# Kernel optimization log

Hardware: AMD Instinct MI355X
Metric: run time of the kernel (lower is better)

The kernel has to match this reference:

```python
import jax, jax.numpy as jnp
import numpy as np
from jax import lax

C = 128
N_HEADS = 4
HEAD_D = C // N_HEADS
EXP = 2  # FFN expansion


def _ln_c(x, g, b, eps):
    # LayerNorm over channel dim of NCHW (equivalent to to_3d -> LN(c) -> to_4d)
    m = jnp.mean(x, axis=1, keepdims=True)
    v = jnp.mean((x - m) ** 2, axis=1, keepdims=True)
    return (x - m) / jnp.sqrt(v + eps) * g[None, :, None, None] + b[None, :, None, None]


def _conv1x1(x, w, b):
    # w: (out, in)
    return jnp.einsum('bchw,oc->bohw', x, w) + b[None, :, None, None]


def _dwconv(x, w, b):
    # depthwise conv, w: (Cg, 1, k, k), stride 1, SAME padding
    y = lax.conv_general_dilated(
        x, w, window_strides=(1, 1), padding='SAME',
        dimension_numbers=('NCHW', 'OIHW', 'NCHW'),
        feature_group_count=x.shape[1])
    return y + b[None, :, None, None]


def setup_inputs() -> dict:
    key = jax.random.key(0)
    ks = jax.random.split(key, 24)
    s = 0.05
    hid = C
    e = EXP * C
    inp = {
        'feats1': jax.random.normal(ks[0], (2, C, 64, 256), jnp.float32),
        'feats2': jax.random.normal(ks[1], (2, C, 64, 256), jnp.float32),
        # attention norms
        'an_g': jnp.ones((C,), jnp.float32), 'an_b': jnp.zeros((C,), jnp.float32),
        'anc_g': jnp.ones((C,), jnp.float32), 'anc_b': jnp.zeros((C,), jnp.float32),
        # qkv / out 1x1 convs
        'wq': jax.random.normal(ks[2], (hid, C), jnp.float32) * s,
        'bq': jnp.zeros((hid,), jnp.float32),
        'wkv': jax.random.normal(ks[3], (2 * hid, C), jnp.float32) * s,
        'bkv': jnp.zeros((2 * hid,), jnp.float32),
        'wo': jax.random.normal(ks[4], (C, hid), jnp.float32) * s,
        'bo': jnp.zeros((C,), jnp.float32),
        # FFN
        'fn_g': jnp.ones((C,), jnp.float32), 'fn_b': jnp.zeros((C,), jnp.float32),
        'w_in': jax.random.normal(ks[5], (e, C), jnp.float32) * s,
        'b_in': jnp.zeros((e,), jnp.float32),
        'w_dw3': jax.random.normal(ks[6], (e, 1, 3, 3), jnp.float32) * s,
        'b_dw3': jnp.zeros((e,), jnp.float32),
        'w_dw5': jax.random.normal(ks[7], (e, 1, 5, 5), jnp.float32) * s,
        'b_dw5': jnp.zeros((e,), jnp.float32),
        'w_dw7': jax.random.normal(ks[8], (e, 1, 7, 7), jnp.float32) * s,
        'b_dw7': jnp.zeros((e,), jnp.float32),
        'w_pw': jax.random.normal(ks[9], (e, 3 * e), jnp.float32) * s,
        'b_pw': jnp.zeros((e,), jnp.float32),
        'w_out': jax.random.normal(ks[10], (C, e), jnp.float32) * s,
        'b_out': jnp.zeros((C,), jnp.float32),
    }
    return inp


def reference(feats1, feats2, an_g, an_b, anc_g, anc_b, wq, bq, wkv, bkv, wo, bo,
              fn_g, fn_b, w_in, b_in, w_dw3, b_dw3, w_dw5, b_dw5, w_dw7, b_dw7,
              w_pw, b_pw, w_out, b_out):
    eps = 1e-6
    hid = C
    n, d = N_HEADS, HEAD_D
    scale = d ** (-0.5)

    # bi-directional cross attention: doubled batch
    cat1 = jnp.concatenate([feats1, feats2], axis=0)  # (B, C, H, W)
    cat2 = jnp.concatenate([feats2, feats1], axis=0)
    B, _, H, W = cat1.shape

    # pre-norm (separate norms for query and context streams)
    x1 = _ln_c(cat1, an_g, an_b, eps)
    x2 = _ln_c(cat2, anc_g, anc_b, eps)

    q = _conv1x1(x1, wq, bq)                     # (B, hid, H, W)
    kv = _conv1x1(x2, wkv, bkv)
    k, v = kv[:, :hid], kv[:, hid:]

    qh = q.reshape(B, n, d, H, W)
    kh = k.reshape(B, n, d, H, W)
    vh = v.reshape(B, n, d, H, W)

    # per-row (epipolar) attention over width
    sim = jnp.einsum('bndhi,bndhj->bnhij', qh, kh) * scale  # (B, n, H, W, W)
    # sink competition renorm
    attn = jax.nn.softmax(sim, axis=-1) + eps
    attn = attn / jnp.sum(attn, axis=-1, keepdims=True)

    o = jnp.einsum('bnhij,bndhj->bndhi', attn, vh).reshape(B, hid, H, W)
    o = _conv1x1(o, wo, bo)
    cat1 = cat1 + o

    # multiscale depthwise-conv FFN (receptive_aug='conv')
    y = _ln_c(cat1, fn_g, fn_b, 1e-5)
    y = jax.nn.silu(_conv1x1(y, w_in, b_in))     # (B, 2C, H, W)
    f3 = _dwconv(y, w_dw3, b_dw3)
    f5 = _dwconv(y, w_dw5, b_dw5)
    f7 = _dwconv(y, w_dw7, b_dw7)
    y = y + jax.nn.silu(_conv1x1(jnp.concatenate([f3, f5, f7], axis=1), w_pw, b_pw))
    y = _conv1x1(y, w_out, b_out)
    cat1 = cat1 + y

    half = B // 2
    return cat1[:half], cat1[half:]
```

## Files before the change

### kernel.cpp

```cpp
#include <hip/hip_runtime.h>

typedef unsigned short u16;
typedef unsigned int u32;

constexpr int H_ = 64;
constexpr int W_ = 256;
constexpr int HW_ = H_ * W_;

typedef __bf16 bf16x8 __attribute__((ext_vector_type(8)));
typedef float f32x4 __attribute__((ext_vector_type(4)));

__device__ __forceinline__ float bf2f(u16 v) { return __uint_as_float(((u32)v) << 16); }
__device__ __forceinline__ u16 f2bf(float f) {
  u32 x = __float_as_uint(f);
  u32 r = (x + 0x7fffu + ((x >> 16) & 1u)) >> 16;
  return (u16)r;
}
__device__ __forceinline__ float lo2f(u32 p) { return __uint_as_float(p << 16); }
__device__ __forceinline__ float hi2f(u32 p) { return __uint_as_float(p & 0xffff0000u); }
__device__ __forceinline__ void unpack8(uint4 v, float* f) {
  f[0] = lo2f(v.x); f[1] = hi2f(v.x);
  f[2] = lo2f(v.y); f[3] = hi2f(v.y);
  f[4] = lo2f(v.z); f[5] = hi2f(v.z);
  f[6] = lo2f(v.w); f[7] = hi2f(v.w);
}
__device__ __forceinline__ bf16x8 as_bf16x8(uint4 v) {
  union { uint4 u; bf16x8 b; } x; x.u = v; return x.b;
}
__device__ __forceinline__ int swz(int p, int c) { return c ^ (((p >> 3) & 3) << 3); }

constexpr int NT = 26;
constexpr int ELEMS_PER_BLK = 4096;
struct CvtArgs {
  const void* src[NT];
  u32 dst_off[NT];
  u32 n[NT];
  u32 blk_start[NT];
};

__global__ void convert_all(CvtArgs a, u16* __restrict__ dst) {
  const u32 bid = blockIdx.x;
  int ti = 0;
#pragma unroll
  for (int k = 1; k < NT; ++k) if (a.blk_start[k] <= bid) ti = k;
  const u32 e0 = (bid - a.blk_start[ti]) * ELEMS_PER_BLK;
  const u32 n = a.n[ti];
  u32 hi = e0 + ELEMS_PER_BLK; if (hi > n) hi = n;
  const float* sp = (const float*)a.src[ti];
  u16* d = dst + a.dst_off[ti];
  for (u32 i = e0 + threadIdx.x; i < hi; i += 256) d[i] = f2bf(sp[i]);
}

template <int CIN, int COUT>
__launch_bounds__(256)
__global__ void gemm1x1_ln(const u16* __restrict__ xA, const u16* __restrict__ xB,
                           const u16* __restrict__ w, const u16* __restrict__ bias,
                           const u16* __restrict__ lng, const u16* __restrict__ lnb,
                           float lneps, u16* __restrict__ out) {
  constexpr int POS = 64;
  constexpr int PITCH = CIN + 8;
  constexpr int MT = COUT / 64;
  __shared__ __align__(16) u16 xs[POS * PITCH];
  __shared__ float red1[256], red2[256], stm[64], str[64];
  const int t = threadIdx.x;
  const int b = blockIdx.y;
  const int pos0 = blockIdx.x * POS;

  const u16* basep = (b >= 2) ? xB : xA;
  const int bb = (b < 2) ? b : b - 2;
  const u16* xb16 = basep + (size_t)bb * CIN * HW_;

  constexpr int NLOAD = CIN * POS / 8;
  for (int idx = t; idx < NLOAD; idx += 256) {
    const int c = idx / (POS / 8);
    const int p8 = (idx % (POS / 8)) * 8;
    uint4 v = *(const uint4*)(xb16 + (size_t)c * HW_ + pos0 + p8);
    const int csw = swz(p8, c);
    u16* row = xs + p8 * PITCH + csw;
    row[0]         = (u16)v.x; row[PITCH]     = (u16)(v.x >> 16);
    row[2 * PITCH] = (u16)v.y; row[3 * PITCH] = (u16)(v.y >> 16);
    row[4 * PITCH] = (u16)v.z; row[5 * PITCH] = (u16)(v.z >> 16);
    row[6 * PITCH] = (u16)v.w; row[7 * PITCH] = (u16)(v.w >> 16);
  }
  __syncthreads();

  {
    const int p = t & 63, part = t >> 6;
    const int xorp = ((p >> 3) & 3) << 3;
    float s = 0.f, sq = 0.f;
#pragma unroll
    for (int k = 0; k < 32; k += 8) {
      uint4 v = *(const uint4*)(xs + p * PITCH + ((part * 32 + k) ^ xorp));
      float f[8]; unpack8(v, f);
#pragma unroll
      for (int j = 0; j < 8; ++j) { s += f[j]; sq += f[j] * f[j]; }
    }
    red1[part * 64 + p] = s; red2[part * 64 + p] = sq;
    __syncthreads();
    if (t < 64) {
      float ss = red1[t] + red1[64 + t] + red1[128 + t] + red1[192 + t];
      float qq = red2[t] + red2[64 + t] + red2[128 + t] + red2[192 + t];
      float m = ss * (1.0f / CIN);
      float var = qq * (1.0f / CIN) - m * m;
      var = var < 0.f ? 0.f : var;
      stm[t] = m; str[t] = rsqrtf(var + lneps);
    }
    __syncthreads();
    const float m = stm[p], r = str[p];
#pragma unroll
    for (int k = 0; k < 32; k += 8) {
      const int c = part * 32 + k;
      uint4 v = *(const uint4*)(xs + p * PITCH + (c ^ xorp));
      float f[8]; unpack8(v, f);
      u32 pk[4];
#pragma unroll
      for (int j = 0; j < 8; j += 2) {
        float g0 = bf2f(lng[c + j]), be0 = bf2f(lnb[c + j]);
        float g1 = bf2f(lng[c + j + 1]), be1 = bf2f(lnb[c + j + 1]);
        u16 lo = f2bf((f[j] - m) * r * g0 + be0);
        u16 hi = f2bf((f[j + 1] - m) * r * g1 + be1);
        pk[j >> 1] = (u32)lo | ((u32)hi << 16);
      }
      uint4 ov; ov.x = pk[0]; ov.y = pk[1]; ov.z = pk[2]; ov.w = pk[3];
      *(uint4*)(xs + p * PITCH + (c ^ xorp)) = ov;
    }
    __syncthreads();
  }

  const int lane = t & 63, wv = t >> 6;
  const int lo16 = lane & 15, quad = lane >> 4;
  const int orow0 = wv * MT * 16;
  const int qrow = quad * 4;

  f32x4 acc[MT][4];
#pragma unroll
  for (int mt = 0; mt < MT; ++mt) {
#pragma unroll
    for (int r = 0; r < 4; ++r) {
      const float bv = bf2f(bias[orow0 + mt * 16 + qrow + r]);
#pragma unroll
      for (int nt = 0; nt < 4; ++nt) acc[mt][nt][r] = bv;
    }
  }

  const u16* xb[4];
#pragma unroll
  for (int nt = 0; nt < 4; ++nt) {
    const int row = nt * 16 + lo16;
    xb[nt] = xs + row * PITCH + (quad * 8 ^ ((((row >> 3) & 3)) << 3));
  }
  const u16* wl = w + (size_t)(orow0 + lo16) * CIN + quad * 8;

#pragma unroll 2
  for (int kc = 0; kc < CIN / 32; ++kc) {
    const int c0 = kc * 32;
    bf16x8 bfr[4];
#pragma unroll
    for (int nt = 0; nt < 4; ++nt)
      bfr[nt] = as_bf16x8(*(const uint4*)(xb[nt] + c0));
#pragma unroll
    for (int mt = 0; mt < MT; ++mt) {
      bf16x8 afr = as_bf16x8(*(const uint4*)(wl + (size_t)mt * 16 * CIN + c0));
#pragma unroll
      for (int nt = 0; nt < 4; ++nt)
        acc[mt][nt] = __builtin_amdgcn_mfma_f32_16x16x32_bf16(afr, bfr[nt], acc[mt][nt], 0, 0, 0);
    }
  }

#pragma unroll
  for (int mt = 0; mt < MT; ++mt) {
#pragma unroll
    for (int nt = 0; nt < 4; ++nt) {
#pragma unroll
      for (int r = 0; r < 4; ++r) {
        const int o = orow0 + mt * 16 + qrow + r;
        const int p = pos0 + nt * 16 + lo16;
        out[((size_t)b * COUT + o) * HW_ + p] = f2bf(acc[mt][nt][r]);
      }
    }
  }
}

__launch_bounds__(256)
__global__ void attn_mfma(const u16* __restrict__ qb, const u16* __restrict__ kvb,
                          u16* __restrict__ ob) {
  constexpr int PA = 40;
  constexpr int PJ = 264;
  __shared__ __align__(16) u16 kT[256 * PA];
  __shared__ __align__(16) u16 vT[32 * PJ];
  __shared__ __align__(16) u16 PlO[4 * 16 * PJ];
  const int t = threadIdx.x;
  const int h = blockIdx.x, n = blockIdx.y, b = blockIdx.z;
  const size_t qbase = ((size_t)(b * 128 + n * 32)) * HW_ + (size_t)h * W_;
  const size_t kbase = ((size_t)(b * 256 + n * 32)) * HW_ + (size_t)h * W_;
  const size_t vbase = ((size_t)(b * 256 + 128 + n * 32)) * HW_ + (size_t)h * W_;

#pragma unroll
  for (int d8 = 0; d8 < 4; ++d8) {
    u32 pk[4];
#pragma unroll
    for (int j = 0; j < 4; ++j) {
      u32 lo = kvb[kbase + (size_t)(d8 * 8 + 2 * j) * HW_ + t];
      u32 hi = kvb[kbase + (size_t)(d8 * 8 + 2 * j + 1) * HW_ + t];
      pk[j] = lo | (hi << 16);
    }
    *(uint4*)(kT + t * PA + d8 * 8) = make_uint4(pk[0], pk[1], pk[2], pk[3]);
  }
#pragma unroll
  for (int k = 0; k < 16; ++k) {
    const int idx = k * 256 + t;
    const int d = idx >> 7, p2 = (idx & 127) * 2;
    u32 v = *(const u32*)(kvb + vbase + (size_t)d * HW_ + p2);
    *(u32*)(vT + d * PJ + p2) = v;
  }
  __syncthreads();

  const int lane = t & 63, wv = t >> 6;
  const int lo16 = lane & 15, quad = lane >> 4;
  const float scale = 0.17677669529663687f;
  const float renorm = 1.0f / (1.0f + 256.0f * 1e-6f);
  const float addc = 1e-6f * renorm;
  u16* Pw = PlO + wv * 16 * PJ;

  f32x4 oacc[4][2];
  for (int ii = 0; ii < 4; ++ii) {
    const int i0 = ii * 64 + wv * 16;
    u16 qr[8];
#pragma unroll
    for (int j = 0; j < 8; ++j)
      qr[j] = qb[qbase + (size_t)(quad * 8 + j) * HW_ + i0 + lo16];
    bf16x8 qa;
#pragma unroll
    for (int j = 0; j < 8; ++j) qa[j] = *(__bf16*)&qr[j];
    f32x4 s[16];
#pragma unroll
    for (int jt = 0; jt < 16; ++jt) {
      bf16x8 kb = as_bf16x8(*(const uint4*)(kT + (jt * 16 + lo16) * PA + quad * 8));
      f32x4 z = {0.f, 0.f, 0.f, 0.f};
      s[jt] = __builtin_amdgcn_mfma_f32_16x16x32_bf16(qa, kb, z, 0, 0, 0);
    }
#pragma unroll
    for (int r = 0; r < 4; ++r) {
      float sum = 0.f;
#pragma unroll
      for (int jt = 0; jt < 16; ++jt) {
        float e = __expf(s[jt][r] * scale);
        s[jt][r] = e; sum += e;
      }
#pragma unroll
      for (int off = 1; off <= 8; off <<= 1) sum += __shfl_xor(sum, off, 64);
      const float inv2 = renorm / sum;
#pragma unroll
      for (int jt = 0; jt < 16; ++jt)
        Pw[(quad * 4 + r) * PJ + jt * 16 + lo16] = f2bf(fmaf(s[jt][r], inv2, addc));
    }
    f32x4 o0 = {0.f, 0.f, 0.f, 0.f}, o1 = {0.f, 0.f, 0.f, 0.f};
#pragma unroll
    for (int kt = 0; kt < 8; ++kt) {
      bf16x8 pa = as_bf16x8(*(const uint4*)(Pw + lo16 * PJ + kt * 32 + quad * 8));
      bf16x8 v0 = as_bf16x8(*(const uint4*)(vT + lo16 * PJ + kt * 32 + quad * 8));
      bf16x8 v1 = as_bf16x8(*(const uint4*)(vT + (16 + lo16) * PJ + kt * 32 + quad * 8));
      o0 = __builtin_amdgcn_mfma_f32_16x16x32_bf16(pa, v0, o0, 0, 0, 0);
      o1 = __builtin_amdgcn_mfma_f32_16x16x32_bf16(pa, v1, o1, 0, 0, 0);
    }
    oacc[ii][0] = o0; oacc[ii][1] = o1;
  }
  __syncthreads();
  u16* Ob = PlO;
#pragma unroll
  for (int ii = 0; ii < 4; ++ii) {
    const int i0 = ii * 64 + wv * 16;
#pragma unroll
    for (int r = 0; r < 4; ++r) {
      Ob[(i0 + quad * 4 + r) * PA + lo16] = f2bf(oacc[ii][0][r]);
      Ob[(i0 + quad * 4 + r) * PA + 16 + lo16] = f2bf(oacc[ii][1][r]);
    }
  }
  __syncthreads();
  for (int d = 0; d < 32; ++d) ob[qbase + (size_t)d * HW_ + t] = Ob[t * PA + d];
}

__launch_bounds__(256)
__global__ void fused_proj_ffn(const u16* __restrict__ obf,
                               const u16* __restrict__ wo, const u16* __restrict__ bo_,
                               const float* __restrict__ f1, const float* __restrict__ f2,
                               const u16* __restrict__ fng, const u16* __restrict__ fnb,
                               const u16* __restrict__ w_in, const u16* __restrict__ b_in,
                               u16* __restrict__ cat1b, u16* __restrict__ yb) {
  constexpr int PITCH = 136;
  __shared__ __align__(16) u16 xs[64 * PITCH];
  __shared__ float red1[256], red2[256], stm[64], str[64];
  const int t = threadIdx.x;
  const int b = blockIdx.y;
  const int pos0 = blockIdx.x * 64;
  const u16* xb16 = obf + (size_t)b * 128 * HW_;

  for (int idx = t; idx < 1024; idx += 256) {
    const int c = idx >> 3, p8 = (idx & 7) * 8;
    uint4 v = *(const uint4*)(xb16 + (size_t)c * HW_ + pos0 + p8);
    const int csw = swz(p8, c);
    u16* row = xs + p8 * PITCH + csw;
    row[0]         = (u16)v.x; row[PITCH]     = (u16)(v.x >> 16);
    row[2 * PITCH] = (u16)v.y; row[3 * PITCH] = (u16)(v.y >> 16);
    row[4 * PITCH] = (u16)v.z; row[5 * PITCH] = (u16)(v.z >> 16);
    row[6 * PITCH] = (u16)v.w; row[7 * PITCH] = (u16)(v.w >> 16);
  }
  __syncthreads();

  const int lane = t & 63, wv = t >> 6;
  const int lo16 = lane & 15, quad = lane >> 4, qrow = quad * 4;
  const u16* xb[4];
#pragma unroll
  for (int nt = 0; nt < 4; ++nt) {
    const int row = nt * 16 + lo16;
    xb[nt] = xs + row * PITCH + (quad * 8 ^ ((((row >> 3) & 3)) << 3));
  }

  const int orow0 = wv * 32;
  f32x4 acc1[2][4];
#pragma unroll
  for (int mt = 0; mt < 2; ++mt)
#pragma unroll
    for (int r = 0; r < 4; ++r) {
      const float bv = bf2f(bo_[orow0 + mt * 16 + qrow + r]);
#pragma unroll
      for (int nt = 0; nt < 4; ++nt) acc1[mt][nt][r] = bv;
    }
  const u16* wl1 = wo + (size_t)(orow0 + lo16) * 128 + quad * 8;
#pragma unroll
  for (int kc = 0; kc < 4; ++kc) {
    const int c0 = kc * 32;
    bf16x8 bfr[4];
#pragma unroll
    for (int nt = 0; nt < 4; ++nt) bfr[nt] = as_bf16x8(*(const uint4*)(xb[nt] + c0));
#pragma unroll
    for (int mt = 0; mt < 2; ++mt) {
      bf16x8 afr = as_bf16x8(*(const uint4*)(wl1 + (size_t)mt * 16 * 128 + c0));
#pragma unroll
      for (int nt = 0; nt < 4; ++nt)
        acc1[mt][nt] = __builtin_amdgcn_mfma_f32_16x16x32_bf16(afr, bfr[nt], acc1[mt][nt], 0, 0, 0);
    }
  }
  __syncthreads();

  {
    const int bl = (b < 2) ? b : b - 2;
    const float* rb = (b < 2) ? f1 : f2;
#pragma unroll
    for (int mt = 0; mt < 2; ++mt)
#pragma unroll
      for (int nt = 0; nt < 4; ++nt)
#pragma unroll
        for (int r = 0; r < 4; ++r) {
          const int o = orow0 + mt * 16 + qrow + r;
          const int p = nt * 16 + lo16;
          float v = acc1[mt][nt][r] + rb[((size_t)bl * 128 + o) * HW_ + pos0 + p];
          const u16 bv = f2bf(v);
          cat1b[((size_t)b * 128 + o) * HW_ + pos0 + p] = bv;
          xs[p * PITCH + swz(p, o)] = bv;
        }
  }
  __syncthreads();

  {
    const int p = t & 63, part = t >> 6;
    const int xorp = ((p >> 3) & 3) << 3;
    float s = 0.f, sq = 0.f;
#pragma unroll
    for (int k = 0; k < 32; k += 8) {
      uint4 v = *(const uint4*)(xs + p * PITCH + ((part * 32 + k) ^ xorp));
      float f[8]; unpack8(v, f);
#pragma unroll
      for (int j = 0; j < 8; ++j) { s += f[j]; sq += f[j] * f[j]; }
    }
    red1[part * 64 + p] = s; red2[part * 64 + p] = sq;
    __syncthreads();
    if (t < 64) {
      float ss = red1[t] + red1[64 + t] + red1[128 + t] + red1[192 + t];
      float qq = red2[t] + red2[64 + t] + red2[128 + t] + red2[192 + t];
      float m = ss * (1.0f / 128.0f);
      float var = qq * (1.0f / 128.0f) - m * m;
      var = var < 0.f ? 0.f : var;
      stm[t] = m; str[t] = rsqrtf(var + 1e-5f);
    }
    __syncthreads();
    const float m = stm[p], r = str[p];
#pragma unroll
    for (int k = 0; k < 32; k += 8) {
      const int c = part * 32 + k;
      uint4 v = *(const uint4*)(xs + p * PITCH + (c ^ xorp));
      float f[8]; unpack8(v, f);
      u32 pk[4];
#pragma unroll
      for (int j = 0; j < 8; j += 2) {
        float g0 = bf2f(fng[c + j]), be0 = bf2f(fnb[c + j]);
        float g1 = bf2f(fng[c + j + 1]), be1 = bf2f(fnb[c + j + 1]);
        u16 lo = f2bf((f[j] - m) * r * g0 + be0);
        u16 hi = f2bf((f[j + 1] - m) * r * g1 + be1);
        pk[j >> 1] = (u32)lo | ((u32)hi << 16);
      }
      uint4 ov; ov.x = pk[0]; ov.y = pk[1]; ov.z = pk[2]; ov.w = pk[3];
      *(uint4*)(xs + p * PITCH + (c ^ xorp)) = ov;
    }
    __syncthreads();
  }

  const int orow2 = wv * 64;
  f32x4 acc2[4][4];
#pragma unroll
  for (int mt = 0; mt < 4; ++mt)
#pragma unroll
    for (int r = 0; r < 4; ++r) {
      const float bv = bf2f(b_in[orow2 + mt * 16 + qrow + r]);
#pragma unroll
      for (int nt = 0; nt < 4; ++nt) acc2[mt][nt][r] = bv;
    }
  const u16* wl2 = w_in + (size_t)(orow2 + lo16) * 128 + quad * 8;
#pragma unroll
  for (int kc = 0; kc < 4; ++kc) {
    const int c0 = kc * 32;
    bf16x8 bfr[4];
#pragma unroll
    for (int nt = 0; nt < 4; ++nt) bfr[nt] = as_bf16x8(*(const uint4*)(xb[nt] + c0));
#pragma unroll
    for (int mt = 0; mt < 4; ++mt) {
      bf16x8 afr = as_bf16x8(*(const uint4*)(wl2 + (size_t)mt * 16 * 128 + c0));
#pragma unroll
      for (int nt = 0; nt < 4; ++nt)
        acc2[mt][nt] = __builtin_amdgcn_mfma_f32_16x16x32_bf16(afr, bfr[nt], acc2[mt][nt], 0, 0, 0);
    }
  }
#pragma unroll
  for (int mt = 0; mt < 4; ++mt)
#pragma unroll
    for (int nt = 0; nt < 4; ++nt)
#pragma unroll
      for (int r = 0; r < 4; ++r) {
        const int o = orow2 + mt * 16 + qrow + r;
        const int p = nt * 16 + lo16;
        float v = acc2[mt][nt][r];
        v = v / (1.0f + __expf(-v));
        yb[((size_t)b * 256 + o) * HW_ + pos0 + p] = f2bf(v);
      }
}

__launch_bounds__(512, 4)
__global__ void fused_pw_out(const u16* __restrict__ fbase, size_t f_stride,
                             const u16* __restrict__ w_pw, const u16* __restrict__ b_pw,
                             const u16* __restrict__ yb,
                             const u16* __restrict__ w_out, const u16* __restrict__ b_out,
                             const u16* __restrict__ cat1b, float* __restrict__ outp,
                             int b_off) {
  constexpr int SP = 136;
  constexpr int P2 = 264;
  constexpr int NCHK = 6;
  __shared__ __align__(16) u16 sbuf[2][64 * SP];
  u16* y2 = &sbuf[0][0];

  const int t = threadIdx.x;
  const int bo2 = (int)blockIdx.y + b_off;
  const int pos0 = blockIdx.x * 64;
  const u16* xf = fbase + (size_t)blockIdx.y * f_stride;

  const int lane = t & 63, wv = t >> 6;
  const int lo16 = lane & 15, quad = lane >> 4, qrow = quad * 4;

  const int c_s0 = t >> 3;
  const int c_s1 = c_s0 + 64;
  const int p8_s = (t & 7) * 8;
  const size_t g_off = pos0 + p8_s;

  uint4 pf0, pf1;
  pf0 = *(const uint4*)(xf + (size_t)c_s0 * HW_ + g_off);
  pf1 = *(const uint4*)(xf + (size_t)c_s1 * HW_ + g_off);
  {
    u16* r0 = sbuf[0] + p8_s * SP + swz(p8_s, c_s0);
    r0[0]      = (u16)pf0.x; r0[SP]     = (u16)(pf0.x >> 16);
    r0[2 * SP] = (u16)pf0.y; r0[3 * SP] = (u16)(pf0.y >> 16);
    r0[4 * SP] = (u16)pf0.z; r0[5 * SP] = (u16)(pf0.z >> 16);
    r0[6 * SP] = (u16)pf0.w; r0[7 * SP] = (u16)(pf0.w >> 16);
    u16* r1 = sbuf[0] + p8_s * SP + swz(p8_s, c_s1);
    r1[0]      = (u16)pf1.x; r1[SP]     = (u16)(pf1.x >> 16);
    r1[2 * SP] = (u16)pf1.y; r1[3 * SP] = (u16)(pf1.y >> 16);
    r1[4 * SP] = (u16)pf1.z; r1[5 * SP] = (u16)(pf1.z >> 16);
    r1[6 * SP] = (u16)pf1.w; r1[7 * SP] = (u16)(pf1.w >> 16);
  }
  pf0 = *(const uint4*)(xf + (size_t)(128 + c_s0) * HW_ + g_off);
  pf1 = *(const uint4*)(xf + (size_t)(128 + c_s1) * HW_ + g_off);

  const int orow1 = wv * 32;
  f32x4 acc[2][4];
#pragma unroll
  for (int mt = 0; mt < 2; ++mt)
#pragma unroll
    for (int r = 0; r < 4; ++r) {
      const float bv = bf2f(b_pw[orow1 + mt * 16 + qrow + r]);
#pragma unroll
      for (int nt = 0; nt < 4; ++nt) acc[mt][nt][r] = bv;
    }
  int xoff[4];
#pragma unroll
  for (int nt = 0; nt < 4; ++nt) {
    const int row = nt * 16 + lo16;
    xoff[nt] = row * SP + (quad * 8 ^ ((((row >> 3) & 3)) << 3));
  }
  const u16* wl1 = w_pw + (size_t)(orow1 + lo16) * 768 + quad * 8;

  __syncthreads();

  for (int ch = 0; ch < NCHK; ++ch) {
    if (ch + 1 < NCHK) {
      u16* dst = sbuf[(ch + 1) & 1];
      u16* r0 = dst + p8_s * SP + swz(p8_s, c_s0);
      r0[0]      = (u16)pf0.x; r0[SP]     = (u16)(pf0.x >> 16);
      r0[2 * SP] = (u16)pf0.y; r0[3 * SP] = (u16)(pf0.y >> 16);
      r0[4 * SP] = (u16)pf0.z; r0[5 * SP] = (u16)(pf0.z >> 16);
      r0[6 * SP] = (u16)pf0.w; r0[7 * SP] = (u16)(pf0.w >> 16);
      u16* r1 = dst + p8_s * SP + swz(p8_s, c_s1);
      r1[0]      = (u16)pf1.x; r1[SP]     = (u16)(pf1.x >> 16);
      r1[2 * SP] = (u16)pf1.y; r1[3 * SP] = (u16)(pf1.y >> 16);
      r1[4 * SP] = (u16)pf1.z; r1[5 * SP] = (u16)(pf1.z >> 16);
      r1[6 * SP] = (u16)pf1.w; r1[7 * SP] = (u16)(pf1.w >> 16);
    }
    if (ch + 2 < NCHK) {
      pf0 = *(const uint4*)(xf + (size_t)((ch + 2) * 128 + c_s0) * HW_ + g_off);
      pf1 = *(const uint4*)(xf + (size_t)((ch + 2) * 128 + c_s1) * HW_ + g_off);
    }
    const u16* xs = sbuf[ch & 1];
    const u16* wch = wl1 + ch * 128;
#pragma unroll
    for (int kc = 0; kc < 4; ++kc) {
      const int c0 = kc * 32;
      bf16x8 bfr[4];
#pragma unroll
      for (int nt = 0; nt < 4; ++nt)
        bfr[nt] = as_bf16x8(*(const uint4*)(xs + xoff[nt] + c0));
#pragma unroll
      for (int mt = 0; mt < 2; ++mt) {
        bf16x8 afr = as_bf16x8(*(const uint4*)(wch + (size_t)mt * 16 * 768 + c0));
#pragma unroll
        for (int nt = 0; nt < 4; ++nt)
          acc[mt][nt] = __builtin_amdgcn_mfma_f32_16x16x32_bf16(afr, bfr[nt], acc[mt][nt], 0, 0, 0);
      }
    }
    __syncthreads();
  }

#pragma unroll
  for (int mt = 0; mt < 2; ++mt)
#pragma unroll
    for (int nt = 0; nt < 4; ++nt)
#pragma unroll
      for (int r = 0; r < 4; ++r) {
        const int o = orow1 + mt * 16 + qrow + r;
        const int p = nt * 16 + lo16;
        float v = acc[mt][nt][r];
        v = v / (1.0f + __expf(-v));
        v += bf2f(yb[((size_t)bo2 * 256 + o) * HW_ + pos0 + p]);
        y2[p * P2 + swz(p, o)] = f2bf(v);
      }
  __syncthreads();

  int x2off[4];
#pragma unroll
  for (int nt = 0; nt < 4; ++nt) {
    const int row = nt * 16 + lo16;
    x2off[nt] = row * P2 + (quad * 8 ^ ((((row >> 3) & 3)) << 3));
  }
  const int orow2 = wv * 16;
  f32x4 acc2[4];
#pragma unroll
  for (int r = 0; r < 4; ++r) {
    const float bv = bf2f(b_out[orow2 + qrow + r]);
#pragma unroll
    for (int nt = 0; nt < 4; ++nt) acc2[nt][r] = bv;
  }
  const u16* wl2 = w_out + (size_t)(orow2 + lo16) * 256 + quad * 8;
#pragma unroll
  for (int kc = 0; kc < 8; ++kc) {
    const int c0 = kc * 32;
    bf16x8 bfr[4];
#pragma unroll
    for (int nt = 0; nt < 4; ++nt) bfr[nt] = as_bf16x8(*(const uint4*)(y2 + x2off[nt] + c0));
    bf16x8 afr = as_bf16x8(*(const uint4*)(wl2 + c0));
#pragma unroll
    for (int nt = 0; nt < 4; ++nt)
      acc2[nt] = __builtin_amdgcn_mfma_f32_16x16x32_bf16(afr, bfr[nt], acc2[nt], 0, 0, 0);
  }
#pragma unroll
  for (int nt = 0; nt < 4; ++nt)
#pragma unroll
    for (int r = 0; r < 4; ++r) {
      const int o = orow2 + qrow + r;
      const int p = nt * 16 + lo16;
      const size_t gidx = ((size_t)bo2 * 128 + o) * HW_ + pos0 + p;
      outp[gidx] = acc2[nt][r] + bf2f(cat1b[gidx]);
    }
}

__launch_bounds__(256)
__global__ void dwconv_kernel(const u16* __restrict__ yB,
                              const u16* __restrict__ w3, const u16* __restrict__ b3,
                              const u16* __restrict__ w5, const u16* __restrict__ b5,
                              const u16* __restrict__ w7, const u16* __restrict__ b7,
                              u16* __restrict__ fB) {
  constexpr int LW = 70, LH = 14, LP = 72;
  __shared__ u16 tile[LH * LP];
  __shared__ float wf7[49], wf5[25], wf3[9];
  const int t = threadIdx.x;
  const int c = blockIdx.y;
  const int bz = blockIdx.z;
  const int tw = blockIdx.x & 3, th = blockIdx.x >> 2;
  const int w0 = tw * 64, h0 = th * 8;
  const u16* src = yB + ((size_t)bz * 256 + c) * HW_;

  if (t < 49) wf7[t] = bf2f(w7[c * 49 + t]);
  if (t >= 64 && t < 89) wf5[t - 64] = bf2f(w5[c * 25 + (t - 64)]);
  if (t >= 96 && t < 105) wf3[t - 96] = bf2f(w3[c * 9 + (t - 96)]);

  for (int idx = t; idx < LH * LW; idx += 256) {
    const int r = idx / LW, cc = idx - r * LW;
    const int gh = h0 + r - 3, gw = w0 + cc - 3;
    u16 v = 0;
    if (gh >= 0 && gh < H_ && gw >= 0 && gw < W_) v = src[gh * W_ + gw];
    tile[r * LP + cc] = v;
  }
  __syncthreads();

  const int x0 = (t & 31) * 2;
  const int hh = t >> 5;
  float a3x = 0.f, a3y = 0.f, a5x = 0.f, a5y = 0.f, a7x = 0.f, a7y = 0.f;
#pragma unroll
  for (int rr = 0; rr < 7; ++rr) {
    const u16* trow = tile + (hh + rr) * LP + x0;
    float f[10];
#pragma unroll
    for (int k = 0; k < 5; ++k) {
      u32 v = *(const u32*)(trow + 2 * k);
      f[2 * k] = lo2f(v); f[2 * k + 1] = hi2f(v);
    }
#pragma unroll
    for (int dx = 0; dx < 7; ++dx) {
      const float wv = wf7[rr * 7 + dx];
      a7x += wv * f[dx]; a7y += wv * f[dx + 1];
    }
    if (rr >= 1 && rr <= 5) {
#pragma unroll
      for (int dx = 0; dx < 5; ++dx) {
        const float wv = wf5[(rr - 1) * 5 + dx];
        a5x += wv * f[dx + 1]; a5y += wv * f[dx + 2];
      }
    }
    if (rr >= 2 && rr <= 4) {
#pragma unroll
      for (int dx = 0; dx < 3; ++dx) {
        const float wv = wf3[(rr - 2) * 3 + dx];
        a3x += wv * f[dx + 2]; a3y += wv * f[dx + 3];
      }
    }
  }
  const float B3v = bf2f(b3[c]), B5v = bf2f(b5[c]), B7v = bf2f(b7[c]);
  const size_t o0 = (size_t)bz * 768 * HW_ + (size_t)c * HW_ + (size_t)(h0 + hh) * W_ + (w0 + x0);
  *(u32*)(fB + o0) = (u32)f2bf(a3x + B3v) | ((u32)f2bf(a3y + B3v) << 16);
  *(u32*)(fB + o0 + (size_t)256 * HW_) = (u32)f2bf(a5x + B5v) | ((u32)f2bf(a5y + B5v) << 16);
  *(u32*)(fB + o0 + (size_t)512 * HW_) = (u32)f2bf(a7x + B7v) | ((u32)f2bf(a7y + B7v) << 16);
}

extern "C" void kernel_launch(void* const* d_in, const int* in_sizes, int n_in,
                              void* d_out, int out_size, void* d_ws, size_t ws_size,
                              hipStream_t stream) {
  (void)out_size; (void)n_in;
  char* ws = (char*)d_ws;
  const size_t MB = 1ull << 20;

  u16* arena = (u16*)ws;
  CvtArgs ca;
  u32 off = 0, blk = 0;
  u32 aoff[NT];
  for (int i = 0; i < NT; ++i) {
    ca.src[i] = d_in[i];
    ca.n[i] = (u32)in_sizes[i];
    ca.dst_off[i] = off;
    aoff[i] = off;
    ca.blk_start[i] = blk;
    off += (ca.n[i] + 15u) & ~15u;
    blk += (ca.n[i] + ELEMS_PER_BLK - 1) / ELEMS_PER_BLK;
  }
  const u32 total_blocks = blk;

  const u16* f1c   = arena + aoff[0];
  const u16* f2c   = arena + aoff[1];
  const u16* an_g  = arena + aoff[2];
  const u16* an_b  = arena + aoff[3];
  const u16* anc_g = arena + aoff[4];
  const u16* anc_b = arena + aoff[5];
  const u16* wq    = arena + aoff[6];
  const u16* bq    = arena + aoff[7];
  const u16* wkv   = arena + aoff[8];
  const u16* bkv   = arena + aoff[9];
  const u16* wo    = arena + aoff[10];
  const u16* bo_   = arena + aoff[11];
  const u16* fn_g  = arena + aoff[12];
  const u16* fn_b  = arena + aoff[13];
  const u16* w_in  = arena + aoff[14];
  const u16* b_in  = arena + aoff[15];
  const u16* w3    = arena + aoff[16];
  const u16* b3    = arena + aoff[17];
  const u16* w5    = arena + aoff[18];
  const u16* b5    = arena + aoff[19];
  const u16* w7    = arena + aoff[20];
  const u16* b7    = arena + aoff[21];
  const u16* w_pw  = arena + aoff[22];
  const u16* b_pw  = arena + aoff[23];
  const u16* w_out = arena + aoff[24];
  const u16* b_out = arena + aoff[25];

  u16* cat1b  = (u16*)(ws + 18 * MB);
  u16* qb     = (u16*)(ws + 34 * MB);
  u16* kvb    = (u16*)(ws + 50 * MB);
  u16* obf    = (u16*)(ws + 82 * MB);
  u16* yb     = (u16*)(ws + 34 * MB);
  u16* fbuf   = (u16*)(ws + 66 * MB);
  float* outp = (float*)d_out;
  const bool big = ws_size >= 168 * MB;

  dim3 blk256(256);
  dim3 blk512(512);
  convert_all<<<total_blocks, 256, 0, stream>>>(ca, arena);

  gemm1x1_ln<128, 128><<<dim3(HW_ / 64, 4), blk256, 0, stream>>>(
      f1c, f2c, wq, bq, an_g, an_b, 1e-6f, qb);
  gemm1x1_ln<128, 256><<<dim3(HW_ / 64, 4), blk256, 0, stream>>>(
      f2c, f1c, wkv, bkv, anc_g, anc_b, 1e-6f, kvb);
  attn_mfma<<<dim3(64, 4, 4), blk256, 0, stream>>>(qb, kvb, obf);
  fused_proj_ffn<<<dim3(HW_ / 64, 4), blk256, 0, stream>>>(
      obf, wo, bo_, (const float*)d_in[0], (const float*)d_in[1],
      fn_g, fn_b, w_in, b_in, cat1b, yb);
  if (big) {
    dwconv_kernel<<<dim3(32, 256, 4), blk256, 0, stream>>>(yb, w3, b3, w5, b5, w7, b7, fbuf);
    fused_pw_out<<<dim3(HW_ / 64, 4), blk512, 0, stream>>>(
        fbuf, (size_t)768 * HW_, w_pw, b_pw, yb, w_out, b_out, cat1b, outp, 0);
  } else {
    for (int b = 0; b < 4; ++b) {
      dwconv_kernel<<<dim3(32, 256, 1), blk256, 0, stream>>>(
          yb + (size_t)b * 256 * HW_, w3, b3, w5, b5, w7, b7, fbuf);
      fused_pw_out<<<dim3(HW_ / 64, 1), blk512, 0, stream>>>(
          fbuf, 0, w_pw, b_pw, yb, w_out, b_out, cat1b, outp, b);
    }
  }
}
```

Baseline: 376.9 us.

## Widen depthwise conv tiles to full rows with 8 outputs per thread

The depthwise 3/5/7 conv kernel now tiles full 256-wide rows (8 rows per block) and stores the halo tile in shared memory as fp32 instead of bf16. Each thread computes 8 adjacent outputs per scale instead of 2, using vectorized float4 LDS reads of input and padded weights, and writes 16-byte stores. This cuts halo overhead, per-element bf16 unpacking and LDS traffic per output, and improves store width. In exchange the grid shrinks fourfold, register pressure rises with 24 accumulators, and the fp32 tile uses more LDS, which may lower occupancy.

After: 438.9 us. +16.4%, slower.

```diff
diff --git a/kernel.cpp b/kernel.cpp
--- a/kernel.cpp
+++ b/kernel.cpp
@@ -604,66 +604,99 @@
                               const u16* __restrict__ w5, const u16* __restrict__ b5,
                               const u16* __restrict__ w7, const u16* __restrict__ b7,
                               u16* __restrict__ fB) {
-  constexpr int LW = 70, LH = 14, LP = 72;
-  __shared__ u16 tile[LH * LP];
-  __shared__ float wf7[49], wf5[25], wf3[9];
+  constexpr int TP = 264;
+  __shared__ __align__(16) float tile[14 * TP];
+  __shared__ __align__(16) float wf7p[56];
+  __shared__ __align__(16) float wf5p[40];
+  __shared__ __align__(16) float wf3p[12];
   const int t = threadIdx.x;
   const int c = blockIdx.y;
   const int bz = blockIdx.z;
-  const int tw = blockIdx.x & 3, th = blockIdx.x >> 2;
-  const int w0 = tw * 64, h0 = th * 8;
+  const int h0 = blockIdx.x * 8;
   const u16* src = yB + ((size_t)bz * 256 + c) * HW_;
 
-  if (t < 49) wf7[t] = bf2f(w7[c * 49 + t]);
-  if (t >= 64 && t < 89) wf5[t - 64] = bf2f(w5[c * 25 + (t - 64)]);
-  if (t >= 96 && t < 105) wf3[t - 96] = bf2f(w3[c * 9 + (t - 96)]);
-
-  for (int idx = t; idx < LH * LW; idx += 256) {
-    const int r = idx / LW, cc = idx - r * LW;
-    const int gh = h0 + r - 3, gw = w0 + cc - 3;
-    u16 v = 0;
-    if (gh >= 0 && gh < H_ && gw >= 0 && gw < W_) v = src[gh * W_ + gw];
-    tile[r * LP + cc] = v;
-  }
-  __syncthreads();
-
-  const int x0 = (t & 31) * 2;
+  if (t < 56) {
+    const int rr = t >> 3, dx = t & 7;
+    wf7p[t] = (dx < 7) ? bf2f(w7[c * 49 + rr * 7 + dx]) : 0.f;
+  } else if (t >= 64 && t < 104) {
+    const int i = t - 64, rr = i >> 3, dx = i & 7;
+    wf5p[i] = (dx < 5) ? bf2f(w5[c * 25 + rr * 5 + dx]) : 0.f;
+  } else if (t >= 112 && t < 124) {
+    const int i = t - 112, rr = i >> 2, dx = i & 3;
+    wf3p[i] = (dx < 3) ? bf2f(w3[c * 9 + rr * 3 + dx]) : 0.f;
+  }
+
+  for (int idx = t; idx < 14 * TP; idx += 256) {
+    const int r = idx / TP, x = idx - r * TP;
+    const int gh = h0 + r - 3, gw = x - 3;
+    float v = 0.f;
+    if (gh >= 0 && gh < H_ && gw >= 0 && gw < W_) v = bf2f(src[gh * W_ + gw]);
+    tile[idx] = v;
+  }
+  __syncthreads();
+
   const int hh = t >> 5;
-  float a3x = 0.f, a3y = 0.f, a5x = 0.f, a5y = 0.f, a7x = 0.f, a7y = 0.f;
+  const int x0 = (t & 31) * 8;
+  float a3[8], a5[8], a7[8];
+#pragma unroll
+  for (int j = 0; j < 8; ++j) { a3[j] = 0.f; a5[j] = 0.f; a7[j] = 0.f; }
+
 #pragma unroll
   for (int rr = 0; rr < 7; ++rr) {
-    const u16* trow = tile + (hh + rr) * LP + x0;
-    float f[10];
-#pragma unroll
-    for (int k = 0; k < 5; ++k) {
-      u32 v = *(const u32*)(trow + 2 * k);
-      f[2 * k] = lo2f(v); f[2 * k + 1] = hi2f(v);
-    }
-#pragma unroll
-    for (int dx = 0; dx < 7; ++dx) {
-      const float wv = wf7[rr * 7 + dx];
-      a7x += wv * f[dx]; a7y += wv * f[dx + 1];
+    const float* trow = tile + (hh + rr) * TP + x0;
+    float f[16];
+#pragma unroll
+    for (int k = 0; k < 4; ++k) {
+      f32x4 v = *(const f32x4*)(trow + 4 * k);
+      f[4 * k] = v[0]; f[4 * k + 1] = v[1]; f[4 * k + 2] = v[2]; f[4 * k + 3] = v[3];
+    }
+    {
+      f32x4 wa = *(const f32x4*)(wf7p + rr * 8);
+      f32x4 wb = *(const f32x4*)(wf7p + rr * 8 + 4);
+      const float w0 = wa[0], w1 = wa[1], w2 = wa[2], w3v = wa[3];
+      const float w4 = wb[0], w5v = wb[1], w6 = wb[2];
+#pragma unroll
+      for (int j = 0; j < 8; ++j) {
+        float s = fmaf(w0, f[j], fmaf(w1, f[j + 1], fmaf(w2, f[j + 2], fmaf(w3v, f[j + 3],
+                  fmaf(w4, f[j + 4], fmaf(w5v, f[j + 5], w6 * f[j + 6]))))));
+        a7[j] += s;
+      }
     }
     if (rr >= 1 && rr <= 5) {
-#pragma unroll
-      for (int dx = 0; dx < 5; ++dx) {
-        const float wv = wf5[(rr - 1) * 5 + dx];
-        a5x += wv * f[dx + 1]; a5y += wv * f[dx + 2];
+      f32x4 wa = *(const f32x4*)(wf5p + (rr - 1) * 8);
+      f32x4 wb = *(const f32x4*)(wf5p + (rr - 1) * 8 + 4);
+      const float w0 = wa[0], w1 = wa[1], w2 = wa[2], w3v = wa[3], w4 = wb[0];
+#pragma unroll
+      for (int j = 0; j < 8; ++j) {
+        float s = fmaf(w0, f[j + 1], fmaf(w1, f[j + 2], fmaf(w2, f[j + 3],
+                  fmaf(w3v, f[j + 4], w4 * f[j + 5]))));
+        a5[j] += s;
       }
     }
     if (rr >= 2 && rr <= 4) {
-#pragma unroll
-      for (int dx = 0; dx < 3; ++dx) {
-        const float wv = wf3[(rr - 2) * 3 + dx];
-        a3x += wv * f[dx + 2]; a3y += wv * f[dx + 3];
-      }
-    }
-  }
+      f32x4 wv = *(const f32x4*)(wf3p + (rr - 2) * 4);
+      const float w0 = wv[0], w1 = wv[1], w2 = wv[2];
+#pragma unroll
+      for (int j = 0; j < 8; ++j) {
+        float s = fmaf(w0, f[j + 2], fmaf(w1, f[j + 3], w2 * f[j + 4]));
+        a3[j] += s;
+      }
+    }
+  }
+
   const float B3v = bf2f(b3[c]), B5v = bf2f(b5[c]), B7v = bf2f(b7[c]);
-  const size_t o0 = (size_t)bz * 768 * HW_ + (size_t)c * HW_ + (size_t)(h0 + hh) * W_ + (w0 + x0);
-  *(u32*)(fB + o0) = (u32)f2bf(a3x + B3v) | ((u32)f2bf(a3y + B3v) << 16);
-  *(u32*)(fB + o0 + (size_t)256 * HW_) = (u32)f2bf(a5x + B5v) | ((u32)f2bf(a5y + B5v) << 16);
-  *(u32*)(fB + o0 + (size_t)512 * HW_) = (u32)f2bf(a7x + B7v) | ((u32)f2bf(a7y + B7v) << 16);
+  uint4 p3, p5, p7;
+  u32* p3w = (u32*)&p3; u32* p5w = (u32*)&p5; u32* p7w = (u32*)&p7;
+#pragma unroll
+  for (int j = 0; j < 8; j += 2) {
+    p3w[j >> 1] = (u32)f2bf(a3[j] + B3v) | ((u32)f2bf(a3[j + 1] + B3v) << 16);
+    p5w[j >> 1] = (u32)f2bf(a5[j] + B5v) | ((u32)f2bf(a5[j + 1] + B5v) << 16);
+    p7w[j >> 1] = (u32)f2bf(a7[j] + B7v) | ((u32)f2bf(a7[j + 1] + B7v) << 16);
+  }
+  const size_t o0 = (size_t)bz * 768 * HW_ + (size_t)c * HW_ + (size_t)(h0 + hh) * W_ + x0;
+  *(uint4*)(fB + o0) = p3;
+  *(uint4*)(fB + o0 + (size_t)256 * HW_) = p5;
+  *(uint4*)(fB + o0 + (size_t)512 * HW_) = p7;
 }
 
 extern "C" void kernel_launch(void* const* d_in, const int* in_sizes, int n_in,
@@ -737,12 +770,12 @@
       obf, wo, bo_, (const float*)d_in[0], (const float*)d_in[1],
       fn_g, fn_b, w_in, b_in, cat1b, yb);
   if (big) {
-    dwconv_kernel<<<dim3(32, 256, 4), blk256, 0, stream>>>(yb, w3, b3, w5, b5, w7, b7, fbuf);
+    dwconv_kernel<<<dim3(8, 256, 4), blk256, 0, stream>>>(yb, w3, b3, w5, b5, w7, b7, fbuf);
     fused_pw_out<<<dim3(HW_ / 64, 4), blk512, 0, stream>>>(
         fbuf, (size_t)768 * HW_, w_pw, b_pw, yb, w_out, b_out, cat1b, outp, 0);
   } else {
     for (int b = 0; b < 4; ++b) {
-      dwconv_kernel<<<dim3(32, 256, 1), blk256, 0, stream>>>(
+      dwconv_kernel<<<dim3(8, 256, 1), blk256, 0, stream>>>(
           yb + (size_t)b * 256 * HW_, w3, b3, w5, b5, w7, b7, fbuf);
       fused_pw_out<<<dim3(HW_ / 64, 1), blk512, 0, stream>>>(
           fbuf, 0, w_pw, b_pw, yb, w_out, b_out, cat1b, outp, b);
```
